# Performance work log

Hardware: AMD Instinct MI355X
Metric: run time of the kernel (lower is better)

Reference implementation:

```python
import jax, jax.numpy as jnp
import numpy as np


def _gcn(G, A, x, W, b):
    # G: (K,N,N) chebyshev supports, A: (B,N,N) attention, x: (B,N,p)
    s = jnp.einsum('kij,bjp->bkip', G, x)          # graph conv per cheb order
    s = jnp.einsum('bij,bkjp->bikp', A, s)         # attention bmm, -> (B,N,K,p)
    B, N, K, p = s.shape
    s = s.reshape(B, N, K * p)                     # concat over k (k-major blocks)
    return s @ W + b


def setup_inputs() -> dict:
    key = jax.random.key(0)
    ks = jax.random.split(key, 8)
    B, T, N, C = 16, 12, 1024, 1
    K, H = 3, 64
    din = C + H  # 65
    x = jax.random.normal(ks[0], (B, T, N, C), dtype=jnp.float32)
    G = jax.random.normal(ks[1], (K, N, N), dtype=jnp.float32) / np.sqrt(N)
    A = jax.random.uniform(ks[2], (B, N, N), dtype=jnp.float32) / N
    W_gate = jax.random.normal(ks[3], (K * din, 2 * H), dtype=jnp.float32) * 0.02
    b_gate = jnp.zeros((2 * H,), dtype=jnp.float32)
    W_update = jax.random.normal(ks[4], (K * din, H), dtype=jnp.float32) * 0.02
    b_update = jnp.zeros((H,), dtype=jnp.float32)
    W_dec = jax.random.normal(ks[5], (H, 12 * 1), dtype=jnp.float32) * 0.02
    b_dec = jnp.zeros((12,), dtype=jnp.float32)
    return {"x": x, "G": G, "A": A, "W_gate": W_gate, "b_gate": b_gate,
            "W_update": W_update, "b_update": b_update, "W_dec": W_dec, "b_dec": b_dec}


def reference(x, G, A, W_gate, b_gate, W_update, b_update, W_dec, b_dec):
    B, T, N, _ = x.shape
    H = W_update.shape[1]
    out_steps, output_dim = 12, 1

    def step(h, xt):
        combined = jnp.concatenate([xt, h], axis=-1)              # (B,N,din)
        zr = jax.nn.sigmoid(_gcn(G, A, combined, W_gate, b_gate))  # (B,N,2H)
        z, r = zr[..., :H], zr[..., H:]
        cand = jnp.concatenate([xt, r * h], axis=-1)
        hc = jnp.tanh(_gcn(G, A, cand, W_update, b_update))
        h_new = z * hc + (1.0 - z) * h
        return h_new, None

    h0 = jnp.zeros((B, N, H), dtype=x.dtype)
    h_last, _ = jax.lax.scan(step, h0, jnp.swapaxes(x, 0, 1))      # scan over T
    out = h_last @ W_dec + b_dec                                   # (B,N,out_steps*output_dim)
    out = out.reshape(B, N, out_steps, output_dim)
    return jnp.transpose(out, (0, 2, 1, 3))                        # (B,out_steps,N,output_dim)
```

## Files before the change

kernel.cpp:

```cpp
#include <hip/hip_runtime.h>
#include <hip/hip_cooperative_groups.h>

namespace cg = cooperative_groups;

#define B_  16
#define T_  12
#define N_  1024
#define K_  3
#define H_  64
#define DIN 65
#define KH  192
#define OG  128

typedef _Float16 f16x4 __attribute__((ext_vector_type(4)));
typedef _Float16 f16x8 __attribute__((ext_vector_type(8)));
typedef float    f32x4 __attribute__((ext_vector_type(4)));

static const size_t OFF_H   = 0;
static const size_t OFF_ZF  = 1048576;
static const size_t OFF_S2  = 2097152;
static const size_t OFF_HTA = 2686976;
static const size_t OFF_HTB = 3211264;
static const size_t OFF_S1  = 3735552;
static const size_t OFF_WGT = 4030464;
static const size_t OFF_WUT = 4042752;
static const size_t OFF_WX  = 4048896;
static const size_t OFF_GT  = 4049472;
static const size_t OFF_AG  = 5622336;
static const size_t OFF_AF  = 30788160;

__global__ __launch_bounds__(256) void k_pre(const float* __restrict__ A,
                                             const float* __restrict__ G,
                                             const float* __restrict__ x,
                                             const float* __restrict__ Wg,
                                             const float* __restrict__ Wu,
                                             _Float16* __restrict__ Af,
                                             _Float16* __restrict__ GfT,
                                             _Float16* __restrict__ S1,
                                             _Float16* __restrict__ wghT,
                                             _Float16* __restrict__ wuhT,
                                             float* __restrict__ wx) {
    __shared__ __align__(16) char smem[23040];
    int bx0 = blockIdx.x, tid = threadIdx.x;
    if (bx0 < 96) {
        int bx = bx0;
        int nh = bx & 1, it = (bx >> 1) & 15, kk = bx >> 5;
        int i0 = it * 64, m0 = nh * 96;
        _Float16 (*sA)[72] = reinterpret_cast<_Float16(*)[72]>(smem);
        _Float16 (*sB)[72] = reinterpret_cast<_Float16(*)[72]>(smem + 9216);
        int wid = tid >> 6, ln = tid & 15, kl = (tid & 63) >> 4;
        const float* Gk = G + (size_t)kk * N_ * N_;
        f32x4 acc[6];
        #pragma unroll
        for (int n = 0; n < 6; ++n) acc[n] = (f32x4){0.f, 0.f, 0.f, 0.f};
        for (int kc = 0; kc < N_; kc += 64) {
            #pragma unroll
            for (int it2 = 0; it2 < 4; ++it2) {
                int idx = it2 * 256 + tid; int row = idx >> 4, c4 = (idx & 15) * 4;
                float4 g = *(const float4*)&Gk[(size_t)(i0 + row) * N_ + kc + c4];
                f16x4 hv = {(_Float16)g.x, (_Float16)g.y, (_Float16)g.z, (_Float16)g.w};
                *(f16x4*)&sA[row][c4] = hv;
            }
            #pragma unroll
            for (int it2 = 0; it2 < 6; ++it2) {
                int idx = it2 * 256 + tid; int row = idx >> 4, c4 = (idx & 15) * 4;
                float4 g = *(const float4*)&x[(size_t)(m0 + row) * N_ + kc + c4];
                f16x4 hv = {(_Float16)g.x, (_Float16)g.y, (_Float16)g.z, (_Float16)g.w};
                *(f16x4*)&sB[row][c4] = hv;
            }
            __syncthreads();
            #pragma unroll
            for (int ks = 0; ks < 4; ++ks) {
                int ko = ks * 16 + kl * 4;
                f16x4 a = *(const f16x4*)&sA[wid * 16 + ln][ko];
                #pragma unroll
                for (int n = 0; n < 6; ++n) {
                    f16x4 b = *(const f16x4*)&sB[n * 16 + ln][ko];
                    acc[n] = __builtin_amdgcn_mfma_f32_16x16x16f16(a, b, acc[n], 0, 0, 0);
                }
            }
            __syncthreads();
        }
        #pragma unroll
        for (int n = 0; n < 6; ++n) {
            int m = m0 + n * 16 + ln;
            #pragma unroll
            for (int r = 0; r < 4; ++r) {
                int i = i0 + wid * 16 + kl * 4 + r;
                S1[(((size_t)kk * 192 + m) << 10) + i] = (_Float16)acc[n][r];
            }
        }
    } else if (bx0 < 864) {
        int bx = bx0 - 96;
        int kk = bx >> 8, rem = bx & 255, ti = rem >> 4, tj = rem & 15;
        int i0 = ti * 64, j0 = tj * 64;
        _Float16 (*s)[72] = reinterpret_cast<_Float16(*)[72]>(smem);
        int r = tid >> 2, cb = (tid & 3) * 16;
        const float* Gp = G + ((size_t)kk << 20) + ((size_t)(i0 + r) << 10) + j0 + cb;
        #pragma unroll
        for (int q = 0; q < 4; ++q) {
            float4 v = *(const float4*)&Gp[q * 4];
            f16x4 hv = {(_Float16)v.x, (_Float16)v.y, (_Float16)v.z, (_Float16)v.w};
            *(f16x4*)&s[r][cb + q * 4] = hv;
        }
        __syncthreads();
        alignas(16) _Float16 tmp[16];
        #pragma unroll
        for (int q = 0; q < 16; ++q) tmp[q] = s[cb + q][r];
        _Float16* outp = GfT + ((size_t)kk << 20) + ((size_t)(j0 + r) << 10) + i0 + cb;
        *(f16x8*)&outp[0] = *(f16x8*)&tmp[0];
        *(f16x8*)&outp[8] = *(f16x8*)&tmp[8];
    } else if (bx0 < 1011) {
        const float inv = 1.0f / 1024.0f;
        int idx = (bx0 - 864) * 256 + tid;
        if (idx < 128 * 192) {
            int o = idx / 192, d = idx % 192;
            int k = d / 64, c = d % 64;
            wghT[idx] = (_Float16)(Wg[(size_t)(k * DIN + 1 + c) * OG + o] * inv);
        } else if (idx < 128 * 192 + 64 * 192) {
            int j = idx - 128 * 192;
            int o = j / 192, d = j % 192;
            int k = d / 64, c = d % 64;
            wuhT[j] = (_Float16)(Wu[(size_t)(k * DIN + 1 + c) * H_ + o] * inv);
        } else if (idx < 128 * 192 + 64 * 192 + 576) {
            int j = idx - 128 * 192 - 64 * 192;
            if (j < 384) { int k = j >> 7, o = j & 127; wx[j] = Wg[(size_t)(k * DIN) * OG + o] * inv; }
            else { int j2 = j - 384; int k = j2 >> 6, o = j2 & 63; wx[j] = Wu[(size_t)(k * DIN) * H_ + o] * inv; }
        }
    } else {
        size_t idx = ((size_t)(bx0 - 1011) * 256 + tid) * 8;
        float4 a = *(const float4*)&A[idx];
        float4 c = *(const float4*)&A[idx + 4];
        f16x8 v = {(_Float16)(a.x*1024.f), (_Float16)(a.y*1024.f), (_Float16)(a.z*1024.f), (_Float16)(a.w*1024.f),
                   (_Float16)(c.x*1024.f), (_Float16)(c.y*1024.f), (_Float16)(c.z*1024.f), (_Float16)(c.w*1024.f)};
        *(f16x8*)&Af[idx] = v;
    }
}

__global__ __launch_bounds__(256) void k_main(const _Float16* __restrict__ Af,
                                              const _Float16* __restrict__ GfT,
                                              _Float16* __restrict__ AG,
                                              const _Float16* __restrict__ S1,
                                              float* __restrict__ S2) {
    __shared__ __align__(16) char smem[73728];
    int bx0 = blockIdx.x, tid = threadIdx.x;
    if (bx0 < 256) {
        int bx = bx0; int it = bx & 15, b = bx >> 4; int i0 = it * 64;
        _Float16 (*sA)[72] = reinterpret_cast<_Float16(*)[72]>(smem);
        _Float16 (*sB)[72] = reinterpret_cast<_Float16(*)[72]>(smem + 9216);
        int wid = tid >> 6, ln = tid & 15, kl = (tid & 63) >> 4;
        f32x4 acc[3];
        #pragma unroll
        for (int n = 0; n < 3; ++n) acc[n] = (f32x4){0.f, 0.f, 0.f, 0.f};
        for (int kc = 0; kc < N_; kc += 64) {
            #pragma unroll
            for (int it2 = 0; it2 < 2; ++it2) {
                int idx = it2 * 256 + tid; int row = idx >> 3, c8 = (idx & 7) * 8;
                *(uint4*)&sA[row][c8] = *(const uint4*)&Af[((size_t)b << 20) + ((size_t)(i0 + row) << 10) + kc + c8];
            }
            for (int idx = tid; idx < 288; idx += 256) {
                int row = idx >> 3, c8 = (idx & 7) * 8;
                int kq = row / 12, tq = row - kq * 12;
                *(uint4*)&sB[row][c8] = *(const uint4*)&S1[(((size_t)kq * 192 + b * T_ + tq) << 10) + kc + c8];
            }
            __syncthreads();
            #pragma unroll
            for (int ks = 0; ks < 4; ++ks) {
                int ko = ks * 16 + kl * 4;
                f16x4 a = *(const f16x4*)&sA[wid * 16 + ln][ko];
                #pragma unroll
                for (int n = 0; n < 3; ++n) {
                    f16x4 b = *(const f16x4*)&sB[n * 16 + ln][ko];
                    acc[n] = __builtin_amdgcn_mfma_f32_16x16x16f16(a, b, acc[n], 0, 0, 0);
                }
            }
            __syncthreads();
        }
        #pragma unroll
        for (int n = 0; n < 3; ++n) {
            int col = n * 16 + ln;
            if (col < 36) {
                int kq = col / 12, tq = col - kq * 12;
                #pragma unroll
                for (int r = 0; r < 4; ++r) {
                    int i = i0 + wid * 16 + kl * 4 + r;
                    S2[(((size_t)(b * 3 + kq) * T_ + tq) << 10) + i] = acc[n][r];
                }
            }
        }
    } else {
        int bxr = bx0 - 256;
        int bx = (bxr & 7) * 384 + (bxr >> 3);
        int inst = bx >> 6, tile = bx & 63;
        int b = inst / 3, kk = inst % 3;
        int i0 = (tile >> 3) * 128, j0 = (tile & 7) * 128;
        _Float16 (*sA)[128][72] = reinterpret_cast<_Float16(*)[128][72]>(smem);
        _Float16 (*sB)[128][72] = reinterpret_cast<_Float16(*)[128][72]>(smem + 36864);
        int w = tid >> 6, lane = tid & 63, ln = lane & 15, kg = lane >> 4;
        int mq = (w & 1) * 64, nq = (w >> 1) * 64;
        int srow = tid >> 1, cb = (tid & 1) * 32;
        const _Float16* qa = Af  + ((size_t)b << 20)  + ((size_t)(i0 + srow) << 10) + cb;
        const _Float16* qb = GfT + ((size_t)kk << 20) + ((size_t)(j0 + srow) << 10) + cb;

        f32x4 acc[4][4];
        #pragma unroll
        for (int mt = 0; mt < 4; ++mt)
            #pragma unroll
            for (int nt = 0; nt < 4; ++nt) acc[mt][nt] = (f32x4){0.f, 0.f, 0.f, 0.f};

        f16x8 ra[4], rb[4];
        #pragma unroll
        for (int q = 0; q < 4; ++q) { ra[q] = *(const f16x8*)&qa[q * 8]; rb[q] = *(const f16x8*)&qb[q * 8]; }
        #pragma unroll
        for (int q = 0; q < 4; ++q) {
            *(f16x8*)&sA[0][srow][cb + q * 8] = ra[q];
            *(f16x8*)&sB[0][srow][cb + q * 8] = rb[q];
        }
        __syncthreads();

        for (int tt = 0; tt < 16; ++tt) {
            int cur = tt & 1;
            if (tt < 15) {
                int kn = (tt + 1) * 64;
                #pragma unroll
                for (int q = 0; q < 4; ++q) { ra[q] = *(const f16x8*)&qa[kn + q * 8]; rb[q] = *(const f16x8*)&qb[kn + q * 8]; }
            }
            #pragma unroll
            for (int ks = 0; ks < 2; ++ks) {
                int ko = ks * 32 + kg * 8;
                f16x8 a[4], bfr[4];
                #pragma unroll
                for (int mt = 0; mt < 4; ++mt) a[mt] = *(const f16x8*)&sA[cur][mq + mt * 16 + ln][ko];
                #pragma unroll
                for (int nt = 0; nt < 4; ++nt) bfr[nt] = *(const f16x8*)&sB[cur][nq + nt * 16 + ln][ko];
                #pragma unroll
                for (int mt = 0; mt < 4; ++mt)
                    #pragma unroll
                    for (int nt = 0; nt < 4; ++nt)
                        acc[mt][nt] = __builtin_amdgcn_mfma_f32_16x16x32_f16(a[mt], bfr[nt], acc[mt][nt], 0, 0, 0);
            }
            if (tt < 15) {
                int nb = cur ^ 1;
                #pragma unroll
                for (int q = 0; q < 4; ++q) {
                    *(f16x8*)&sA[nb][srow][cb + q * 8] = ra[q];
                    *(f16x8*)&sB[nb][srow][cb + q * 8] = rb[q];
                }
                __syncthreads();
            }
        }

        _Float16* outp = AG + ((size_t)(b * 3 + kk) << 20);
        #pragma unroll
        for (int mt = 0; mt < 4; ++mt)
            #pragma unroll
            for (int r = 0; r < 4; ++r) {
                int i = i0 + mq + mt * 16 + kg * 4 + r;
                #pragma unroll
                for (int nt = 0; nt < 4; ++nt) {
                    int j = j0 + nq + nt * 16 + ln;
                    outp[((size_t)i << 10) + j] = (_Float16)acc[mt][nt][r];
                }
            }
    }
}

__global__ __launch_bounds__(256, 2) void k_loop(const _Float16* __restrict__ AG,
                                                 _Float16* __restrict__ HtA,
                                                 _Float16* __restrict__ HtB,
                                                 const _Float16* __restrict__ wghT,
                                                 const _Float16* __restrict__ wuhT,
                                                 const float* __restrict__ wx,
                                                 const float* __restrict__ bg,
                                                 const float* __restrict__ bu,
                                                 const float* __restrict__ S2,
                                                 const float* __restrict__ Wd,
                                                 const float* __restrict__ bd,
                                                 float* __restrict__ out) {
    cg::grid_group grid = cg::this_grid();
    int bx = blockIdx.x; int it = bx & 31, b = bx >> 5; int i0 = it * 32;
    __shared__ __align__(16) char smem[46080];
    _Float16 (*sAm)[96][72] = reinterpret_cast<_Float16(*)[96][72]>(smem);
    _Float16 (*sBm)[64][72] = reinterpret_cast<_Float16(*)[64][72]>(smem + 27648);
    _Float16 (*sZ)[200]     = reinterpret_cast<_Float16(*)[200]>(smem);
    _Float16 (*sW)[72]      = reinterpret_cast<_Float16(*)[72]>(smem + 12800);
    __shared__ _Float16 zS[32][64];
    __shared__ float sS2[3][32];
    int tid = threadIdx.x;
    int w = tid >> 6, lane = tid & 63, ln = lane & 15, kg = lane >> 4;

    float h_reg[2][4] = {{0.f, 0.f, 0.f, 0.f}, {0.f, 0.f, 0.f, 0.f}};
    float wxg0[2], wxg1[2], wxg2[2], bgr[2];
    #pragma unroll
    for (int n = 0; n < 2; ++n) {
        int o = w * 32 + n * 16 + ln;
        wxg0[n] = wx[o]; wxg1[n] = wx[128 + o]; wxg2[n] = wx[256 + o]; bgr[n] = bg[o];
    }
    int ou = w * 16 + ln;
    float wxu0 = wx[384 + ou], wxu1 = wx[448 + ou], wxu2 = wx[512 + ou], bur = bu[ou];

    int srow = tid >> 3, sc8 = (tid & 7) * 8;
    const _Float16* pa0 = AG + ((size_t)(b * 3 + 0) << 20) + ((size_t)(i0 + srow) << 10) + sc8;
    const _Float16* pa1 = AG + ((size_t)(b * 3 + 1) << 20) + ((size_t)(i0 + srow) << 10) + sc8;
    const _Float16* pa2 = AG + ((size_t)(b * 3 + 2) << 20) + ((size_t)(i0 + srow) << 10) + sc8;
    size_t hoff0 = ((size_t)b << 16) + ((size_t)srow << 10) + sc8;
    size_t hoff1 = ((size_t)b << 16) + ((size_t)(srow + 32) << 10) + sc8;
    int kbF = (w * 3) >> 2, kbL = (w * 3 + 2) >> 2;

    for (int t = 0; t < T_; ++t) {
        #pragma unroll
        for (int phase = 0; phase < 2; ++phase) {
            const _Float16* HtIn = phase ? HtB : HtA;
            if (tid < 96) { int k = tid >> 5, il = tid & 31; sS2[k][il] = S2[(((size_t)(b * 3 + k) * T_ + t) << 10) + i0 + il]; }
            const _Float16* pb0 = HtIn + hoff0;
            const _Float16* pb1 = HtIn + hoff1;

            f32x4 acc[2][3];
            #pragma unroll
            for (int m = 0; m < 2; ++m)
                #pragma unroll
                for (int n = 0; n < 3; ++n) acc[m][n] = (f32x4){0.f, 0.f, 0.f, 0.f};

            f16x8 rA0 = *(const f16x8*)pa0, rA1 = *(const f16x8*)pa1, rA2 = *(const f16x8*)pa2;
            f16x8 rB0 = *(const f16x8*)pb0, rB1 = *(const f16x8*)pb1;
            *(f16x8*)&sAm[0][srow][sc8] = rA0;
            *(f16x8*)&sAm[0][32 + srow][sc8] = rA1;
            *(f16x8*)&sAm[0][64 + srow][sc8] = rA2;
            *(f16x8*)&sBm[0][srow][sc8] = rB0;
            *(f16x8*)&sBm[0][srow + 32][sc8] = rB1;
            __syncthreads();

            for (int tt = 0; tt < 16; ++tt) {
                int cur = tt & 1;
                if (tt < 15) {
                    int kn = (tt + 1) * 64;
                    rA0 = *(const f16x8*)&pa0[kn]; rA1 = *(const f16x8*)&pa1[kn]; rA2 = *(const f16x8*)&pa2[kn];
                    rB0 = *(const f16x8*)&pb0[kn]; rB1 = *(const f16x8*)&pb1[kn];
                }
                #pragma unroll
                for (int ks = 0; ks < 2; ++ks) {
                    int ko = ks * 32 + kg * 8;
                    f16x8 aF0 = *(const f16x8*)&sAm[cur][kbF * 32 + ln][ko];
                    f16x8 aF1 = *(const f16x8*)&sAm[cur][kbF * 32 + 16 + ln][ko];
                    f16x8 aL0 = *(const f16x8*)&sAm[cur][kbL * 32 + ln][ko];
                    f16x8 aL1 = *(const f16x8*)&sAm[cur][kbL * 32 + 16 + ln][ko];
                    #pragma unroll
                    for (int ni = 0; ni < 3; ++ni) {
                        int ct = w * 3 + ni;
                        f16x8 bb = *(const f16x8*)&sBm[cur][(ct & 3) * 16 + ln][ko];
                        bool late = (ct >> 2) != kbF;
                        f16x8 a0 = late ? aL0 : aF0;
                        f16x8 a1 = late ? aL1 : aF1;
                        acc[0][ni] = __builtin_amdgcn_mfma_f32_16x16x32_f16(a0, bb, acc[0][ni], 0, 0, 0);
                        acc[1][ni] = __builtin_amdgcn_mfma_f32_16x16x32_f16(a1, bb, acc[1][ni], 0, 0, 0);
                    }
                }
                if (tt < 15) {
                    int nb = cur ^ 1;
                    *(f16x8*)&sAm[nb][srow][sc8] = rA0;
                    *(f16x8*)&sAm[nb][32 + srow][sc8] = rA1;
                    *(f16x8*)&sAm[nb][64 + srow][sc8] = rA2;
                    *(f16x8*)&sBm[nb][srow][sc8] = rB0;
                    *(f16x8*)&sBm[nb][srow + 32][sc8] = rB1;
                    __syncthreads();
                }
            }
            __syncthreads();

            #pragma unroll
            for (int m = 0; m < 2; ++m)
                #pragma unroll
                for (int ni = 0; ni < 3; ++ni)
                    #pragma unroll
                    for (int r = 0; r < 4; ++r)
                        sZ[m * 16 + kg * 4 + r][(w * 3 + ni) * 16 + ln] = (_Float16)acc[m][ni][r];

            if (phase == 0) {
                f32x4 e[2][2];
                #pragma unroll
                for (int m = 0; m < 2; ++m)
                    #pragma unroll
                    for (int n = 0; n < 2; ++n) e[m][n] = (f32x4){0.f, 0.f, 0.f, 0.f};
                for (int kc = 0; kc < 192; kc += 64) {
                    #pragma unroll
                    for (int it2 = 0; it2 < 4; ++it2) {
                        int idx = it2 * 256 + tid; int row = idx >> 3, c8 = (idx & 7) * 8;
                        *(f16x8*)&sW[row][c8] = *(const f16x8*)&wghT[(size_t)row * 192 + kc + c8];
                    }
                    __syncthreads();
                    #pragma unroll
                    for (int ks = 0; ks < 4; ++ks) {
                        int ko = ks * 16 + kg * 4;
                        f16x4 az0 = *(const f16x4*)&sZ[ln][kc + ko];
                        f16x4 az1 = *(const f16x4*)&sZ[16 + ln][kc + ko];
                        f16x4 bw0 = *(const f16x4*)&sW[w * 32 + ln][ko];
                        f16x4 bw1 = *(const f16x4*)&sW[w * 32 + 16 + ln][ko];
                        e[0][0] = __builtin_amdgcn_mfma_f32_16x16x16f16(az0, bw0, e[0][0], 0, 0, 0);
                        e[0][1] = __builtin_amdgcn_mfma_f32_16x16x16f16(az0, bw1, e[0][1], 0, 0, 0);
                        e[1][0] = __builtin_amdgcn_mfma_f32_16x16x16f16(az1, bw0, e[1][0], 0, 0, 0);
                        e[1][1] = __builtin_amdgcn_mfma_f32_16x16x16f16(az1, bw1, e[1][1], 0, 0, 0);
                    }
                    __syncthreads();
                }
                #pragma unroll
                for (int n = 0; n < 2; ++n) {
                    int o = w * 32 + n * 16 + ln;
                    if (o < H_) {
                        #pragma unroll
                        for (int m = 0; m < 2; ++m)
                            #pragma unroll
                            for (int r = 0; r < 4; ++r) {
                                int il = m * 16 + kg * 4 + r;
                                float pre = e[m][n][r] + wxg0[n] * sS2[0][il] + wxg1[n] * sS2[1][il] + wxg2[n] * sS2[2][il] + bgr[n];
                                zS[il][o] = (_Float16)(1.0f / (1.0f + expf(-pre)));
                            }
                    } else {
                        int c = o - H_;
                        #pragma unroll
                        for (int m = 0; m < 2; ++m) {
                            f16x4 hold4 = *(const f16x4*)&HtA[((size_t)(b * 64 + c) << 10) + i0 + m * 16 + kg * 4];
                            alignas(8) _Float16 hb[4];
                            #pragma unroll
                            for (int r = 0; r < 4; ++r) {
                                int il = m * 16 + kg * 4 + r;
                                float pre = e[m][n][r] + wxg0[n] * sS2[0][il] + wxg1[n] * sS2[1][il] + wxg2[n] * sS2[2][il] + bgr[n];
                                float v = 1.0f / (1.0f + expf(-pre));
                                hb[r] = (_Float16)(v * (float)hold4[r]);
                            }
                            *(f16x4*)&HtB[((size_t)(b * 64 + c) << 10) + i0 + m * 16 + kg * 4] = *(f16x4*)&hb[0];
                        }
                    }
                }
            } else {
                f32x4 e[2];
                e[0] = (f32x4){0.f, 0.f, 0.f, 0.f};
                e[1] = (f32x4){0.f, 0.f, 0.f, 0.f};
                for (int kc = 0; kc < 192; kc += 64) {
                    #pragma unroll
                    for (int it2 = 0; it2 < 2; ++it2) {
                        int idx = it2 * 256 + tid; int row = idx >> 3, c8 = (idx & 7) * 8;
                        *(f16x8*)&sW[row][c8] = *(const f16x8*)&wuhT[(size_t)row * 192 + kc + c8];
                    }
                    __syncthreads();
                    #pragma unroll
                    for (int ks = 0; ks < 4; ++ks) {
                        int ko = ks * 16 + kg * 4;
                        f16x4 az0 = *(const f16x4*)&sZ[ln][kc + ko];
                        f16x4 az1 = *(const f16x4*)&sZ[16 + ln][kc + ko];
                        f16x4 bw  = *(const f16x4*)&sW[w * 16 + ln][ko];
                        e[0] = __builtin_amdgcn_mfma_f32_16x16x16f16(az0, bw, e[0], 0, 0, 0);
                        e[1] = __builtin_amdgcn_mfma_f32_16x16x16f16(az1, bw, e[1], 0, 0, 0);
                    }
                    __syncthreads();
                }
                #pragma unroll
                for (int m = 0; m < 2; ++m) {
                    alignas(8) _Float16 hb[4];
                    #pragma unroll
                    for (int r = 0; r < 4; ++r) {
                        int il = m * 16 + kg * 4 + r;
                        float pre = e[m][r] + wxu0 * sS2[0][il] + wxu1 * sS2[1][il] + wxu2 * sS2[2][il] + bur;
                        float hc = tanhf(pre);
                        float z = (float)zS[il][ou];
                        float hn = z * hc + (1.0f - z) * h_reg[m][r];
                        h_reg[m][r] = hn;
                        hb[r] = (_Float16)hn;
                    }
                    *(f16x4*)&HtA[((size_t)(b * 64 + ou) << 10) + i0 + m * 16 + kg * 4] = *(f16x4*)&hb[0];
                }
            }
            if (t < T_ - 1 || phase == 0) {
                __threadfence();
                grid.sync();
            }
        }
    }

    __syncthreads();
    float* hF  = (float*)smem;
    float* wds = (float*)(smem + 8192);
    float* bds = (float*)(smem + 11264);
    #pragma unroll
    for (int m = 0; m < 2; ++m)
        #pragma unroll
        for (int r = 0; r < 4; ++r)
            hF[(m * 16 + kg * 4 + r) * 64 + ou] = h_reg[m][r];
    for (int idx = tid; idx < 768; idx += 256) wds[idx] = Wd[idx];
    if (tid < 12) bds[tid] = bd[tid];
    __syncthreads();
    for (int oidx = tid; oidx < 384; oidx += 256) {
        int il = oidx & 31, tt = oidx >> 5;
        float acc = bds[tt];
        #pragma unroll
        for (int c = 0; c < 64; ++c) acc += hF[il * 64 + c] * wds[c * 12 + tt];
        out[(((size_t)(b * T_ + tt)) << 10) + i0 + il] = acc;
    }
}

__global__ __launch_bounds__(256) void k_fzr2(const _Float16* __restrict__ AG,
                                              const _Float16* __restrict__ HtIn,
                                              const _Float16* __restrict__ wghT,
                                              const float* __restrict__ wx,
                                              const float* __restrict__ bg,
                                              const float* __restrict__ S2,
                                              const float* __restrict__ h,
                                              _Float16* __restrict__ zf,
                                              _Float16* __restrict__ HtOut, int t) {
    int bx = blockIdx.x; int it = bx & 63, b = bx >> 6; int i0 = it * 16;
    __shared__ __align__(16) char smem[32256];
    _Float16 (*sA)[48][72] = reinterpret_cast<_Float16(*)[48][72]>(smem);
    _Float16 (*sB)[64][72] = reinterpret_cast<_Float16(*)[64][72]>(smem + 13824);
    _Float16 (*sZ)[200]    = reinterpret_cast<_Float16(*)[200]>(smem);
    _Float16 (*sW)[72]     = reinterpret_cast<_Float16(*)[72]>(smem + 6400);
    __shared__ float sS2[3][16];
    __shared__ float sWX[384];
    __shared__ float sBias[128];
    int tid = threadIdx.x;
    int w = tid >> 6, lane = tid & 63, ln = lane & 15, kg = lane >> 4;
    if (tid < 48) { int k = tid >> 4, il = tid & 15; sS2[k][il] = S2[(((size_t)(b * 3 + k) * T_ + t) << 10) + i0 + il]; }
    for (int q = tid; q < 384; q += 256) sWX[q] = wx[q];
    if (tid < 128) sBias[tid] = bg[tid];

    const _Float16* pA[3]; int c4A[3], rowA[3];
    #pragma unroll
    for (int q = 0; q < 3; ++q) {
        int idx = q * 256 + tid; rowA[q] = idx >> 4; c4A[q] = (idx & 15) * 4;
        int kb = rowA[q] >> 4, rloc = rowA[q] & 15;
        pA[q] = AG + ((size_t)(b * 3 + kb) << 20) + ((size_t)(i0 + rloc) << 10) + c4A[q];
    }
    const _Float16* pB[2]; int c8B[2], rowB[2];
    #pragma unroll
    for (int q = 0; q < 2; ++q) {
        int idx = q * 256 + tid; rowB[q] = idx >> 3; c8B[q] = (idx & 7) * 8;
        pB[q] = HtIn + ((size_t)b << 16) + ((size_t)rowB[q] << 10) + c8B[q];
    }

    f32x4 acc[3];
    #pragma unroll
    for (int n = 0; n < 3; ++n) acc[n] = (f32x4){0.f, 0.f, 0.f, 0.f};

    f16x4 ra[3]; f16x8 rb[2];
    #pragma unroll
    for (int q = 0; q < 3; ++q) ra[q] = *(const f16x4*)pA[q];
    #pragma unroll
    for (int q = 0; q < 2; ++q) rb[q] = *(const f16x8*)pB[q];
    #pragma unroll
    for (int q = 0; q < 3; ++q) *(f16x4*)&sA[0][rowA[q]][c4A[q]] = ra[q];
    #pragma unroll
    for (int q = 0; q < 2; ++q) *(f16x8*)&sB[0][rowB[q]][c8B[q]] = rb[q];
    __syncthreads();

    int kbF = (w * 3) >> 2, kbL = (w * 3 + 2) >> 2;
    for (int tt = 0; tt < 16; ++tt) {
        int cur = tt & 1;
        if (tt < 15) {
            int kn = (tt + 1) * 64;
            #pragma unroll
            for (int q = 0; q < 3; ++q) ra[q] = *(const f16x4*)&pA[q][kn];
            #pragma unroll
            for (int q = 0; q < 2; ++q) rb[q] = *(const f16x8*)&pB[q][kn];
        }
        #pragma unroll
        for (int ks = 0; ks < 2; ++ks) {
            int ko = ks * 32 + kg * 8;
            f16x8 aF = *(const f16x8*)&sA[cur][kbF * 16 + ln][ko];
            f16x8 aL = *(const f16x8*)&sA[cur][kbL * 16 + ln][ko];
            #pragma unroll
            for (int ni = 0; ni < 3; ++ni) {
                int ct = w * 3 + ni;
                f16x8 bb = *(const f16x8*)&sB[cur][(ct & 3) * 16 + ln][ko];
                f16x8 a = ((ct >> 2) != kbF) ? aL : aF;
                acc[ni] = __builtin_amdgcn_mfma_f32_16x16x32_f16(a, bb, acc[ni], 0, 0, 0);
            }
        }
        if (tt < 15) {
            int nb = cur ^ 1;
            #pragma unroll
            for (int q = 0; q < 3; ++q) *(f16x4*)&sA[nb][rowA[q]][c4A[q]] = ra[q];
            #pragma unroll
            for (int q = 0; q < 2; ++q) *(f16x8*)&sB[nb][rowB[q]][c8B[q]] = rb[q];
            __syncthreads();
        }
    }
    __syncthreads();

    #pragma unroll
    for (int ni = 0; ni < 3; ++ni)
        #pragma unroll
        for (int r = 0; r < 4; ++r)
            sZ[kg * 4 + r][(w * 3 + ni) * 16 + ln] = (_Float16)acc[ni][r];

    f32x4 e[2];
    e[0] = (f32x4){0.f, 0.f, 0.f, 0.f};
    e[1] = (f32x4){0.f, 0.f, 0.f, 0.f};
    for (int kc = 0; kc < 192; kc += 64) {
        #pragma unroll
        for (int it2 = 0; it2 < 4; ++it2) {
            int idx = it2 * 256 + tid; int row = idx >> 3, c8 = (idx & 7) * 8;
            *(f16x8*)&sW[row][c8] = *(const f16x8*)&wghT[(size_t)row * 192 + kc + c8];
        }
        __syncthreads();
        #pragma unroll
        for (int ks = 0; ks < 4; ++ks) {
            int ko = ks * 16 + kg * 4;
            f16x4 az  = *(const f16x4*)&sZ[ln][kc + ko];
            f16x4 bw0 = *(const f16x4*)&sW[w * 32 + ln][ko];
            f16x4 bw1 = *(const f16x4*)&sW[w * 32 + 16 + ln][ko];
            e[0] = __builtin_amdgcn_mfma_f32_16x16x16f16(az, bw0, e[0], 0, 0, 0);
            e[1] = __builtin_amdgcn_mfma_f32_16x16x16f16(az, bw1, e[1], 0, 0, 0);
        }
        __syncthreads();
    }

    #pragma unroll
    for (int n = 0; n < 2; ++n) {
        int o = w * 32 + n * 16 + ln;
        float w0 = sWX[o], w1 = sWX[128 + o], w2 = sWX[256 + o], bi = sBias[o];
        if (o < H_) {
            alignas(8) _Float16 zv[4];
            #pragma unroll
            for (int r = 0; r < 4; ++r) {
                int il = kg * 4 + r;
                float pre = e[n][r] + w0 * sS2[0][il] + w1 * sS2[1][il] + w2 * sS2[2][il] + bi;
                zv[r] = (_Float16)(1.0f / (1.0f + expf(-pre)));
            }
            *(f16x4*)&zf[((size_t)(b * 64 + o) << 10) + i0 + kg * 4] = *(f16x4*)&zv[0];
        } else {
            int c = o - H_;
            alignas(8) _Float16 hb[4];
            #pragma unroll
            for (int r = 0; r < 4; ++r) {
                int il = kg * 4 + r;
                float pre = e[n][r] + w0 * sS2[0][il] + w1 * sS2[1][il] + w2 * sS2[2][il] + bi;
                float v = 1.0f / (1.0f + expf(-pre));
                hb[r] = (_Float16)(v * h[((size_t)((b << 10) + i0 + il)) * H_ + c]);
            }
            *(f16x4*)&HtOut[((size_t)(b * 64 + c) << 10) + i0 + kg * 4] = *(f16x4*)&hb[0];
        }
    }
}

__global__ __launch_bounds__(256) void k_fup2(const _Float16* __restrict__ AG,
                                              const _Float16* __restrict__ HtIn,
                                              const _Float16* __restrict__ wuhT,
                                              const float* __restrict__ wx,
                                              const float* __restrict__ bu,
                                              const float* __restrict__ S2,
                                              const _Float16* __restrict__ zf,
                                              float* __restrict__ h,
                                              _Float16* __restrict__ HtOut,
                                              const float* __restrict__ Wd,
                                              const float* __restrict__ bd,
                                              float* __restrict__ out, int t) {
    int bx = blockIdx.x; int it = bx & 63, b = bx >> 6; int i0 = it * 16;
    __shared__ __align__(16) char smem[32256];
    _Float16 (*sA)[48][72] = reinterpret_cast<_Float16(*)[48][72]>(smem);
    _Float16 (*sB)[64][72] = reinterpret_cast<_Float16(*)[64][72]>(smem + 13824);
    _Float16 (*sZ)[200]    = reinterpret_cast<_Float16(*)[200]>(smem);
    _Float16 (*sW)[72]     = reinterpret_cast<_Float16(*)[72]>(smem + 6400);
    __shared__ float sS2[3][16];
    __shared__ float sWX[192];
    __shared__ float sBias[64];
    int tid = threadIdx.x;
    int w = tid >> 6, lane = tid & 63, ln = lane & 15, kg = lane >> 4;
    if (tid < 48) { int k = tid >> 4, il = tid & 15; sS2[k][il] = S2[(((size_t)(b * 3 + k) * T_ + t) << 10) + i0 + il]; }
    if (tid < 192) sWX[tid] = wx[384 + tid];
    if (tid < 64) sBias[tid] = bu[tid];

    const _Float16* pA[3]; int c4A[3], rowA[3];
    #pragma unroll
    for (int q = 0; q < 3; ++q) {
        int idx = q * 256 + tid; rowA[q] = idx >> 4; c4A[q] = (idx & 15) * 4;
        int kb = rowA[q] >> 4, rloc = rowA[q] & 15;
        pA[q] = AG + ((size_t)(b * 3 + kb) << 20) + ((size_t)(i0 + rloc) << 10) + c4A[q];
    }
    const _Float16* pB[2]; int c8B[2], rowB[2];
    #pragma unroll
    for (int q = 0; q < 2; ++q) {
        int idx = q * 256 + tid; rowB[q] = idx >> 3; c8B[q] = (idx & 7) * 8;
        pB[q] = HtIn + ((size_t)b << 16) + ((size_t)rowB[q] << 10) + c8B[q];
    }

    f32x4 acc[3];
    #pragma unroll
    for (int n = 0; n < 3; ++n) acc[n] = (f32x4){0.f, 0.f, 0.f, 0.f};

    f16x4 ra[3]; f16x8 rb[2];
    #pragma unroll
    for (int q = 0; q < 3; ++q) ra[q] = *(const f16x4*)pA[q];
    #pragma unroll
    for (int q = 0; q < 2; ++q) rb[q] = *(const f16x8*)pB[q];
    #pragma unroll
    for (int q = 0; q < 3; ++q) *(f16x4*)&sA[0][rowA[q]][c4A[q]] = ra[q];
    #pragma unroll
    for (int q = 0; q < 2; ++q) *(f16x8*)&sB[0][rowB[q]][c8B[q]] = rb[q];
    __syncthreads();

    int kbF = (w * 3) >> 2, kbL = (w * 3 + 2) >> 2;
    for (int tt = 0; tt < 16; ++tt) {
        int cur = tt & 1;
        if (tt < 15) {
            int kn = (tt + 1) * 64;
            #pragma unroll
            for (int q = 0; q < 3; ++q) ra[q] = *(const f16x4*)&pA[q][kn];
            #pragma unroll
            for (int q = 0; q < 2; ++q) rb[q] = *(const f16x8*)&pB[q][kn];
        }
        #pragma unroll
        for (int ks = 0; ks < 2; ++ks) {
            int ko = ks * 32 + kg * 8;
            f16x8 aF = *(const f16x8*)&sA[cur][kbF * 16 + ln][ko];
            f16x8 aL = *(const f16x8*)&sA[cur][kbL * 16 + ln][ko];
            #pragma unroll
            for (int ni = 0; ni < 3; ++ni) {
                int ct = w * 3 + ni;
                f16x8 bb = *(const f16x8*)&sB[cur][(ct & 3) * 16 + ln][ko];
                f16x8 a = ((ct >> 2) != kbF) ? aL : aF;
                acc[ni] = __builtin_amdgcn_mfma_f32_16x16x32_f16(a, bb, acc[ni], 0, 0, 0);
            }
        }
        if (tt < 15) {
            int nb = cur ^ 1;
            #pragma unroll
            for (int q = 0; q < 3; ++q) *(f16x4*)&sA[nb][rowA[q]][c4A[q]] = ra[q];
            #pragma unroll
            for (int q = 0; q < 2; ++q) *(f16x8*)&sB[nb][rowB[q]][c8B[q]] = rb[q];
            __syncthreads();
        }
    }
    __syncthreads();

    #pragma unroll
    for (int ni = 0; ni < 3; ++ni)
        #pragma unroll
        for (int r = 0; r < 4; ++r)
            sZ[kg * 4 + r][(w * 3 + ni) * 16 + ln] = (_Float16)acc[ni][r];

    f32x4 e = (f32x4){0.f, 0.f, 0.f, 0.f};
    for (int kc = 0; kc < 192; kc += 64) {
        #pragma unroll
        for (int it2 = 0; it2 < 2; ++it2) {
            int idx = it2 * 256 + tid; int row = idx >> 3, c8 = (idx & 7) * 8;
            *(f16x8*)&sW[row][c8] = *(const f16x8*)&wuhT[(size_t)row * 192 + kc + c8];
        }
        __syncthreads();
        #pragma unroll
        for (int ks = 0; ks < 4; ++ks) {
            int ko = ks * 16 + kg * 4;
            f16x4 az = *(const f16x4*)&sZ[ln][kc + ko];
            f16x4 bw = *(const f16x4*)&sW[w * 16 + ln][ko];
            e = __builtin_amdgcn_mfma_f32_16x16x16f16(az, bw, e, 0, 0, 0);
        }
        __syncthreads();
    }

    int o = w * 16 + ln;
    float w0 = sWX[o], w1 = sWX[64 + o], w2 = sWX[128 + o], bi = sBias[o];
    f16x4 z4 = *(const f16x4*)&zf[((size_t)(b * 64 + o) << 10) + i0 + kg * 4];
    alignas(8) _Float16 hb[4];
    float hnv[4];
    #pragma unroll
    for (int r = 0; r < 4; ++r) {
        int il = kg * 4 + r;
        float pre = e[r] + w0 * sS2[0][il] + w1 * sS2[1][il] + w2 * sS2[2][il] + bi;
        float hc = tanhf(pre);
        size_t gi = ((size_t)((b << 10) + i0 + il)) * H_ + o;
        float z = (float)z4[r];
        float hn = z * hc + (1.0f - z) * h[gi];
        h[gi] = hn;
        hnv[r] = hn;
        hb[r] = (_Float16)hn;
    }
    *(f16x4*)&HtOut[((size_t)(b * 64 + o) << 10) + i0 + kg * 4] = *(f16x4*)&hb[0];

    if (t == T_ - 1) {
        __syncthreads();
        float* hF  = (float*)smem;
        float* wds = (float*)(smem + 4096);
        float* bds = (float*)(smem + 7168);
        #pragma unroll
        for (int r = 0; r < 4; ++r) hF[(kg * 4 + r) * 64 + o] = hnv[r];
        for (int idx = tid; idx < 768; idx += 256) wds[idx] = Wd[idx];
        if (tid < 12) bds[tid] = bd[tid];
        __syncthreads();
        for (int oidx = tid; oidx < 192; oidx += 256) {
            int il = oidx & 15, tt2 = oidx >> 4;
            float acc2 = bds[tt2];
            #pragma unroll
            for (int c = 0; c < 64; ++c) acc2 += hF[il * 64 + c] * wds[c * 12 + tt2];
            out[(((size_t)(b * T_ + tt2)) << 10) + i0 + il] = acc2;
        }
    }
}

extern "C" void kernel_launch(void* const* d_in, const int* in_sizes, int n_in,
                              void* d_out, int out_size, void* d_ws, size_t ws_size,
                              hipStream_t stream) {
    const float* x  = (const float*)d_in[0];
    const float* G  = (const float*)d_in[1];
    const float* A  = (const float*)d_in[2];
    const float* Wg = (const float*)d_in[3];
    const float* bg = (const float*)d_in[4];
    const float* Wu = (const float*)d_in[5];
    const float* bu = (const float*)d_in[6];
    const float* Wd = (const float*)d_in[7];
    const float* bd = (const float*)d_in[8];
    float* out = (float*)d_out;
    float* ws  = (float*)d_ws;

    float* h   = ws + OFF_H;
    float* S2  = ws + OFF_S2;
    float* wxb = ws + OFF_WX;
    _Float16* zf   = (_Float16*)(ws + OFF_ZF);
    _Float16* HtA  = (_Float16*)(ws + OFF_HTA);
    _Float16* HtB  = (_Float16*)(ws + OFF_HTB);
    _Float16* S1   = (_Float16*)(ws + OFF_S1);
    _Float16* wghT = (_Float16*)(ws + OFF_WGT);
    _Float16* wuhT = (_Float16*)(ws + OFF_WUT);
    _Float16* GfT  = (_Float16*)(ws + OFF_GT);
    _Float16* AG   = (_Float16*)(ws + OFF_AG);
    _Float16* Af   = (_Float16*)(ws + OFF_AF);

    hipMemsetAsync(h, 0, (size_t)B_ * N_ * H_ * sizeof(float), stream);
    hipMemsetAsync((void*)HtA, 0, (size_t)B_ * N_ * H_ * sizeof(_Float16), stream);
    k_pre<<<9203, 256, 0, stream>>>(A, G, x, Wg, Wu, Af, GfT, S1, wghT, wuhT, wxb);
    k_main<<<3328, 256, 0, stream>>>(Af, GfT, AG, S1, S2);

    int nb = 0;
    hipOccupancyMaxActiveBlocksPerMultiprocessor(&nb, k_loop, 256, 0);
    if (nb >= 2) {
        void* args[] = {(void*)&AG, (void*)&HtA, (void*)&HtB, (void*)&wghT, (void*)&wuhT,
                        (void*)&wxb, (void*)&bg, (void*)&bu, (void*)&S2,
                        (void*)&Wd, (void*)&bd, (void*)&out};
        hipLaunchCooperativeKernel((const void*)k_loop, dim3(512), dim3(256), args, 0, stream);
    } else {
        for (int t = 0; t < T_; ++t) {
            k_fzr2<<<1024, 256, 0, stream>>>(AG, HtA, wghT, wxb, bg, S2, h, zf, HtB, t);
            k_fup2<<<1024, 256, 0, stream>>>(AG, HtB, wuhT, wxb, bu, S2, zf, h, HtA, Wd, bd, out, t);
        }
    }
}
```

Before: 799.8 us.

## Keep gate/update weights in registers and prefetch AG tile across grid sync

In the cooperative recurrent kernel, the gate and update weight fragments are loaded once into registers before the time loop. This replaces the per-step shared-memory staging loops and the barriers around them. The first AG tile is now prefetched before the loop, and each later one is issued just before the grid sync so the load overlaps the barrier. Separately, the S1 precompute in k_pre is split into twice as many smaller tiles to spread the work over more blocks. The trade-off is much higher register pressure, which could cause spills or lower occupancy for a kernel launched at two blocks per SM.

```diff
diff --git a/kernel.cpp b/kernel.cpp
--- a/kernel.cpp
+++ b/kernel.cpp
@@ -42,20 +42,20 @@
                                              float* __restrict__ wx) {
     __shared__ __align__(16) char smem[23040];
     int bx0 = blockIdx.x, tid = threadIdx.x;
-    if (bx0 < 96) {
+    if (bx0 < 192) {
         int bx = bx0;
-        int nh = bx & 1, it = (bx >> 1) & 15, kk = bx >> 5;
-        int i0 = it * 64, m0 = nh * 96;
+        int nh = bx & 1, it = (bx >> 1) & 31, kk = bx >> 6;
+        int i0 = it * 32, m0 = nh * 96;
         _Float16 (*sA)[72] = reinterpret_cast<_Float16(*)[72]>(smem);
-        _Float16 (*sB)[72] = reinterpret_cast<_Float16(*)[72]>(smem + 9216);
+        _Float16 (*sB)[72] = reinterpret_cast<_Float16(*)[72]>(smem + 4608);
         int wid = tid >> 6, ln = tid & 15, kl = (tid & 63) >> 4;
         const float* Gk = G + (size_t)kk * N_ * N_;
-        f32x4 acc[6];
-        #pragma unroll
-        for (int n = 0; n < 6; ++n) acc[n] = (f32x4){0.f, 0.f, 0.f, 0.f};
+        f32x4 acc[3];
+        #pragma unroll
+        for (int n = 0; n < 3; ++n) acc[n] = (f32x4){0.f, 0.f, 0.f, 0.f};
         for (int kc = 0; kc < N_; kc += 64) {
             #pragma unroll
-            for (int it2 = 0; it2 < 4; ++it2) {
+            for (int it2 = 0; it2 < 2; ++it2) {
                 int idx = it2 * 256 + tid; int row = idx >> 4, c4 = (idx & 15) * 4;
                 float4 g = *(const float4*)&Gk[(size_t)(i0 + row) * N_ + kc + c4];
                 f16x4 hv = {(_Float16)g.x, (_Float16)g.y, (_Float16)g.z, (_Float16)g.w};
@@ -72,26 +72,26 @@
             #pragma unroll
             for (int ks = 0; ks < 4; ++ks) {
                 int ko = ks * 16 + kl * 4;
-                f16x4 a = *(const f16x4*)&sA[wid * 16 + ln][ko];
-                #pragma unroll
-                for (int n = 0; n < 6; ++n) {
-                    f16x4 b = *(const f16x4*)&sB[n * 16 + ln][ko];
-                    acc[n] = __builtin_amdgcn_mfma_f32_16x16x16f16(a, b, acc[n], 0, 0, 0);
+                f16x4 a = *(const f16x4*)&sA[(wid & 1) * 16 + ln][ko];
+                #pragma unroll
+                for (int n3 = 0; n3 < 3; ++n3) {
+                    f16x4 b = *(const f16x4*)&sB[((wid >> 1) * 3 + n3) * 16 + ln][ko];
+                    acc[n3] = __builtin_amdgcn_mfma_f32_16x16x16f16(a, b, acc[n3], 0, 0, 0);
                 }
             }
             __syncthreads();
         }
         #pragma unroll
-        for (int n = 0; n < 6; ++n) {
-            int m = m0 + n * 16 + ln;
+        for (int n3 = 0; n3 < 3; ++n3) {
+            int m = m0 + ((wid >> 1) * 3 + n3) * 16 + ln;
             #pragma unroll
             for (int r = 0; r < 4; ++r) {
-                int i = i0 + wid * 16 + kl * 4 + r;
-                S1[(((size_t)kk * 192 + m) << 10) + i] = (_Float16)acc[n][r];
-            }
-        }
-    } else if (bx0 < 864) {
-        int bx = bx0 - 96;
+                int i = i0 + (wid & 1) * 16 + kl * 4 + r;
+                S1[(((size_t)kk * 192 + m) << 10) + i] = (_Float16)acc[n3][r];
+            }
+        }
+    } else if (bx0 < 960) {
+        int bx = bx0 - 192;
         int kk = bx >> 8, rem = bx & 255, ti = rem >> 4, tj = rem & 15;
         int i0 = ti * 64, j0 = tj * 64;
         _Float16 (*s)[72] = reinterpret_cast<_Float16(*)[72]>(smem);
@@ -110,9 +110,9 @@
         _Float16* outp = GfT + ((size_t)kk << 20) + ((size_t)(j0 + r) << 10) + i0 + cb;
         *(f16x8*)&outp[0] = *(f16x8*)&tmp[0];
         *(f16x8*)&outp[8] = *(f16x8*)&tmp[8];
-    } else if (bx0 < 1011) {
+    } else if (bx0 < 1107) {
         const float inv = 1.0f / 1024.0f;
-        int idx = (bx0 - 864) * 256 + tid;
+        int idx = (bx0 - 960) * 256 + tid;
         if (idx < 128 * 192) {
             int o = idx / 192, d = idx % 192;
             int k = d / 64, c = d % 64;
@@ -128,7 +128,7 @@
             else { int j2 = j - 384; int k = j2 >> 6, o = j2 & 63; wx[j] = Wu[(size_t)(k * DIN) * H_ + o] * inv; }
         }
     } else {
-        size_t idx = ((size_t)(bx0 - 1011) * 256 + tid) * 8;
+        size_t idx = ((size_t)(bx0 - 1107) * 256 + tid) * 8;
         float4 a = *(const float4*)&A[idx];
         float4 c = *(const float4*)&A[idx + 4];
         f16x8 v = {(_Float16)(a.x*1024.f), (_Float16)(a.y*1024.f), (_Float16)(a.z*1024.f), (_Float16)(a.w*1024.f),
@@ -283,7 +283,6 @@
     _Float16 (*sAm)[96][72] = reinterpret_cast<_Float16(*)[96][72]>(smem);
     _Float16 (*sBm)[64][72] = reinterpret_cast<_Float16(*)[64][72]>(smem + 27648);
     _Float16 (*sZ)[200]     = reinterpret_cast<_Float16(*)[200]>(smem);
-    _Float16 (*sW)[72]      = reinterpret_cast<_Float16(*)[72]>(smem + 12800);
     __shared__ _Float16 zS[32][64];
     __shared__ float sS2[3][32];
     int tid = threadIdx.x;
@@ -298,6 +297,17 @@
     }
     int ou = w * 16 + ln;
     float wxu0 = wx[384 + ou], wxu1 = wx[448 + ou], wxu2 = wx[512 + ou], bur = bu[ou];
+
+    f16x4 wgr[3][4][2], wur[3][4];
+    #pragma unroll
+    for (int kc = 0; kc < 3; ++kc)
+        #pragma unroll
+        for (int ks = 0; ks < 4; ++ks) {
+            #pragma unroll
+            for (int n = 0; n < 2; ++n)
+                wgr[kc][ks][n] = *(const f16x4*)&wghT[(size_t)(w * 32 + n * 16 + ln) * 192 + kc * 64 + ks * 16 + kg * 4];
+            wur[kc][ks] = *(const f16x4*)&wuhT[(size_t)(w * 16 + ln) * 192 + kc * 64 + ks * 16 + kg * 4];
+        }
 
     int srow = tid >> 3, sc8 = (tid & 7) * 8;
     const _Float16* pa0 = AG + ((size_t)(b * 3 + 0) << 20) + ((size_t)(i0 + srow) << 10) + sc8;
@@ -307,6 +317,8 @@
     size_t hoff1 = ((size_t)b << 16) + ((size_t)(srow + 32) << 10) + sc8;
     int kbF = (w * 3) >> 2, kbL = (w * 3 + 2) >> 2;
 
+    f16x8 rA0 = *(const f16x8*)pa0, rA1 = *(const f16x8*)pa1, rA2 = *(const f16x8*)pa2;
+
     for (int t = 0; t < T_; ++t) {
         #pragma unroll
         for (int phase = 0; phase < 2; ++phase) {
@@ -314,6 +326,7 @@
             if (tid < 96) { int k = tid >> 5, il = tid & 31; sS2[k][il] = S2[(((size_t)(b * 3 + k) * T_ + t) << 10) + i0 + il]; }
             const _Float16* pb0 = HtIn + hoff0;
             const _Float16* pb1 = HtIn + hoff1;
+            f16x8 rB0 = *(const f16x8*)pb0, rB1 = *(const f16x8*)pb1;
 
             f32x4 acc[2][3];
             #pragma unroll
@@ -321,8 +334,6 @@
                 #pragma unroll
                 for (int n = 0; n < 3; ++n) acc[m][n] = (f32x4){0.f, 0.f, 0.f, 0.f};
 
-            f16x8 rA0 = *(const f16x8*)pa0, rA1 = *(const f16x8*)pa1, rA2 = *(const f16x8*)pa2;
-            f16x8 rB0 = *(const f16x8*)pb0, rB1 = *(const f16x8*)pb1;
             *(f16x8*)&sAm[0][srow][sc8] = rA0;
             *(f16x8*)&sAm[0][32 + srow][sc8] = rA1;
             *(f16x8*)&sAm[0][64 + srow][sc8] = rA2;
@@ -374,6 +385,7 @@
                     #pragma unroll
                     for (int r = 0; r < 4; ++r)
                         sZ[m * 16 + kg * 4 + r][(w * 3 + ni) * 16 + ln] = (_Float16)acc[m][ni][r];
+            __syncthreads();
 
             if (phase == 0) {
                 f32x4 e[2][2];
@@ -381,27 +393,19 @@
                 for (int m = 0; m < 2; ++m)
                     #pragma unroll
                     for (int n = 0; n < 2; ++n) e[m][n] = (f32x4){0.f, 0.f, 0.f, 0.f};
-                for (int kc = 0; kc < 192; kc += 64) {
-                    #pragma unroll
-                    for (int it2 = 0; it2 < 4; ++it2) {
-                        int idx = it2 * 256 + tid; int row = idx >> 3, c8 = (idx & 7) * 8;
-                        *(f16x8*)&sW[row][c8] = *(const f16x8*)&wghT[(size_t)row * 192 + kc + c8];
-                    }
-                    __syncthreads();
+                #pragma unroll
+                for (int kc = 0; kc < 3; ++kc)
                     #pragma unroll
                     for (int ks = 0; ks < 4; ++ks) {
-                        int ko = ks * 16 + kg * 4;
-                        f16x4 az0 = *(const f16x4*)&sZ[ln][kc + ko];
-                        f16x4 az1 = *(const f16x4*)&sZ[16 + ln][kc + ko];
-                        f16x4 bw0 = *(const f16x4*)&sW[w * 32 + ln][ko];
-                        f16x4 bw1 = *(const f16x4*)&sW[w * 32 + 16 + ln][ko];
-                        e[0][0] = __builtin_amdgcn_mfma_f32_16x16x16f16(az0, bw0, e[0][0], 0, 0, 0);
-                        e[0][1] = __builtin_amdgcn_mfma_f32_16x16x16f16(az0, bw1, e[0][1], 0, 0, 0);
-                        e[1][0] = __builtin_amdgcn_mfma_f32_16x16x16f16(az1, bw0, e[1][0], 0, 0, 0);
-                        e[1][1] = __builtin_amdgcn_mfma_f32_16x16x16f16(az1, bw1, e[1][1], 0, 0, 0);
+                        int ko = kc * 64 + ks * 16 + kg * 4;
+                        f16x4 az0 = *(const f16x4*)&sZ[ln][ko];
+                        f16x4 az1 = *(const f16x4*)&sZ[16 + ln][ko];
+                        #pragma unroll
+                        for (int n = 0; n < 2; ++n) {
+                            e[0][n] = __builtin_amdgcn_mfma_f32_16x16x16f16(az0, wgr[kc][ks][n], e[0][n], 0, 0, 0);
+                            e[1][n] = __builtin_amdgcn_mfma_f32_16x16x16f16(az1, wgr[kc][ks][n], e[1][n], 0, 0, 0);
+                        }
                     }
-                    __syncthreads();
-                }
                 #pragma unroll
                 for (int n = 0; n < 2; ++n) {
                     int o = w * 32 + n * 16 + ln;
@@ -432,34 +436,26 @@
                     }
                 }
             } else {
-                f32x4 e[2];
-                e[0] = (f32x4){0.f, 0.f, 0.f, 0.f};
-                e[1] = (f32x4){0.f, 0.f, 0.f, 0.f};
-                for (int kc = 0; kc < 192; kc += 64) {
-                    #pragma unroll
-                    for (int it2 = 0; it2 < 2; ++it2) {
-                        int idx = it2 * 256 + tid; int row = idx >> 3, c8 = (idx & 7) * 8;
-                        *(f16x8*)&sW[row][c8] = *(const f16x8*)&wuhT[(size_t)row * 192 + kc + c8];
-                    }
-                    __syncthreads();
+                f32x4 e0 = (f32x4){0.f, 0.f, 0.f, 0.f};
+                f32x4 e1 = (f32x4){0.f, 0.f, 0.f, 0.f};
+                #pragma unroll
+                for (int kc = 0; kc < 3; ++kc)
                     #pragma unroll
                     for (int ks = 0; ks < 4; ++ks) {
-                        int ko = ks * 16 + kg * 4;
-                        f16x4 az0 = *(const f16x4*)&sZ[ln][kc + ko];
-                        f16x4 az1 = *(const f16x4*)&sZ[16 + ln][kc + ko];
-                        f16x4 bw  = *(const f16x4*)&sW[w * 16 + ln][ko];
-                        e[0] = __builtin_amdgcn_mfma_f32_16x16x16f16(az0, bw, e[0], 0, 0, 0);
-                        e[1] = __builtin_amdgcn_mfma_f32_16x16x16f16(az1, bw, e[1], 0, 0, 0);
+                        int ko = kc * 64 + ks * 16 + kg * 4;
+                        f16x4 az0 = *(const f16x4*)&sZ[ln][ko];
+                        f16x4 az1 = *(const f16x4*)&sZ[16 + ln][ko];
+                        e0 = __builtin_amdgcn_mfma_f32_16x16x16f16(az0, wur[kc][ks], e0, 0, 0, 0);
+                        e1 = __builtin_amdgcn_mfma_f32_16x16x16f16(az1, wur[kc][ks], e1, 0, 0, 0);
                     }
-                    __syncthreads();
-                }
                 #pragma unroll
                 for (int m = 0; m < 2; ++m) {
                     alignas(8) _Float16 hb[4];
                     #pragma unroll
                     for (int r = 0; r < 4; ++r) {
                         int il = m * 16 + kg * 4 + r;
-                        float pre = e[m][r] + wxu0 * sS2[0][il] + wxu1 * sS2[1][il] + wxu2 * sS2[2][il] + bur;
+                        float ev = (m == 0) ? e0[r] : e1[r];
+                        float pre = ev + wxu0 * sS2[0][il] + wxu1 * sS2[1][il] + wxu2 * sS2[2][il] + bur;
                         float hc = tanhf(pre);
                         float z = (float)zS[il][ou];
                         float hn = z * hc + (1.0f - z) * h_reg[m][r];
@@ -470,6 +466,7 @@
                 }
             }
             if (t < T_ - 1 || phase == 0) {
+                rA0 = *(const f16x8*)pa0; rA1 = *(const f16x8*)pa1; rA2 = *(const f16x8*)pa2;
                 __threadfence();
                 grid.sync();
             }
@@ -823,7 +820,7 @@
 
     hipMemsetAsync(h, 0, (size_t)B_ * N_ * H_ * sizeof(float), stream);
     hipMemsetAsync((void*)HtA, 0, (size_t)B_ * N_ * H_ * sizeof(_Float16), stream);
-    k_pre<<<9203, 256, 0, stream>>>(A, G, x, Wg, Wu, Af, GfT, S1, wghT, wuhT, wxb);
+    k_pre<<<9299, 256, 0, stream>>>(A, G, x, Wg, Wu, Af, GfT, S1, wghT, wuhT, wxb);
     k_main<<<3328, 256, 0, stream>>>(Af, GfT, AG, S1, S2);
 
     int nb = 0;
```

New measurement: 825.4 us. 3.2% more time.
